# Optimization experiments

Hardware: AMD Instinct MI355X
Metric: run time of the kernel (lower is better)

## Reference

```python
import jax, jax.numpy as jnp
from jax import lax
import numpy as np

T, B, H = 128, 4096, 64

def setup_inputs() -> dict:
    key = jax.random.key(0)
    ks = jax.random.split(key, 7)
    s = 1.0 / np.sqrt(H)
    Hseq = jax.random.normal(ks[0], (T, B, H), dtype=jnp.float32)
    # PyTorch nn.GRU params: weight_ih_l0 [3H,H], weight_hh_l0 [3H,H], biases [3H]; gate order r,z,n
    W_ih = jax.random.uniform(ks[1], (3 * H, H), jnp.float32, -s, s)
    W_hh = jax.random.uniform(ks[2], (3 * H, H), jnp.float32, -s, s)
    b_ih = jax.random.uniform(ks[3], (3 * H,), jnp.float32, -s, s)
    b_hh = jax.random.uniform(ks[4], (3 * H,), jnp.float32, -s, s)
    W_out = jax.random.uniform(ks[5], (1, H), jnp.float32, -s, s)
    b_out = jax.random.uniform(ks[6], (1,), jnp.float32, -s, s)
    return {"Hseq": Hseq, "W_ih": W_ih, "W_hh": W_hh, "b_ih": b_ih, "b_hh": b_hh, "W_out": W_out, "b_out": b_out}

def reference(Hseq, W_ih, W_hh, b_ih, b_hh, W_out, b_out):
    # Precompute all input-side gate projections in one big GEMM: [T,B,3H]
    x_gates = jnp.einsum('tbh,gh->tbg', Hseq, W_ih) + b_ih

    def step(h, xg):
        hg = h @ W_hh.T + b_hh                     # [B,3H]
        xr, xz, xn = jnp.split(xg, 3, axis=-1)
        hr, hz, hn = jnp.split(hg, 3, axis=-1)
        r = jax.nn.sigmoid(xr + hr)
        z = jax.nn.sigmoid(xz + hz)
        n = jnp.tanh(xn + r * hn)
        h_new = (1.0 - z) * n + z * h
        return h_new, None

    h0 = jnp.zeros(Hseq.shape[1:], Hseq.dtype)      # [B,H], PyTorch default h0=0
    last, _ = lax.scan(step, h0, x_gates)           # last hidden == Y[-1]
    return (last @ W_out.T + b_out).squeeze(-1)     # [B]
```

## Files before the change

kernel.cpp:

```cpp
#include <hip/hip_runtime.h>
#include <stdint.h>

#define TT 128
#define BB 4096
#define HH 64
#define BC 16
#define XSTR 196
#define HSTR 72

typedef __attribute__((ext_vector_type(8))) short bf16x8;
typedef __attribute__((ext_vector_type(4))) float f32x4;

static __device__ __forceinline__ short f2bf(float f) {
  uint32_t u = __builtin_bit_cast(uint32_t, f);
  u += 0x7fffu + ((u >> 16) & 1u);
  return (short)(u >> 16);
}
static __device__ __forceinline__ uint32_t cvtpk(float a, float b) {
  uint32_t r;
  asm("v_cvt_pk_bf16_f32 %0, %1, %2" : "=v"(r) : "v"(a), "v"(b));
  return r;
}
static __device__ __forceinline__ float rcpf(float x) { return __builtin_amdgcn_rcpf(x); }
static __device__ __forceinline__ float sigm(float x) { return rcpf(1.0f + __expf(-x)); }
static __device__ __forceinline__ float tanhf_fast(float x) {
  float e = __expf(2.0f * x);
  return 1.0f - 2.0f * rcpf(e + 1.0f);
}

static __device__ __forceinline__ void block_sync_lds() {
  asm volatile("" ::: "memory");
  asm volatile("s_waitcnt lgkmcnt(0)" ::: "memory");
  __builtin_amdgcn_s_barrier();
  asm volatile("" ::: "memory");
}

#define MFMA __builtin_amdgcn_mfma_f32_16x16x32_bf16

__global__ __launch_bounds__(512) void gru_fused(
    const float* __restrict__ Hseq, const float* __restrict__ W_ih,
    const float* __restrict__ W_hh, const float* __restrict__ b_ih,
    const float* __restrict__ b_hh, const float* __restrict__ W_out,
    const float* __restrict__ b_out, float* __restrict__ out) {
  __shared__ __align__(16) short hsh[2][BC][HSTR];
  __shared__ __align__(16) float xgsh[4][BC][XSTR];
  __shared__ float psum[4][BC];

  const int tid = threadIdx.x;
  const int w   = tid >> 6;
  const int gw  = w & 3;
  const bool cons = (w < 4);
  const int l   = tid & 63;
  const int llo = l & 15;
  const int lhi = l >> 4;
  const int k0  = lhi * 8;
  const int bbase = blockIdx.x * BC;
  const f32x4 fz = {0.f, 0.f, 0.f, 0.f};

  for (int i = tid; i < BC * HSTR; i += 512) ((short*)hsh[0])[i] = 0;

  bf16x8 wa[3][2];
  f32x4 biasHN = fz;
  f32x4 biasPR = fz, biasPZ = fz, biasPN = fz;

  if (cons) {
#pragma unroll
    for (int c = 0; c < 3; ++c) {
      const int grow = 16 * gw + 64 * c + llo;
#pragma unroll
      for (int hf = 0; hf < 2; ++hf) {
        const float* q = &W_hh[grow * 64 + hf * 32 + k0];
        bf16x8 b;
#pragma unroll
        for (int i = 0; i < 8; ++i) b[i] = f2bf(q[i]);
        wa[c][hf] = b;
      }
    }
#pragma unroll
    for (int r = 0; r < 4; ++r) biasHN[r] = b_hh[128 + 16 * gw + 4 * lhi + r];
  } else {
#pragma unroll
    for (int c = 0; c < 3; ++c) {
      const int grow = 16 * gw + 64 * c + llo;
#pragma unroll
      for (int hf = 0; hf < 2; ++hf) {
        const float* p = &W_ih[grow * 64 + hf * 32 + k0];
        bf16x8 a;
#pragma unroll
        for (int i = 0; i < 8; ++i) a[i] = f2bf(p[i]);
        wa[c][hf] = a;
      }
    }
#pragma unroll
    for (int r = 0; r < 4; ++r) {
      const int j = 16 * gw + 4 * lhi + r;
      biasPR[r] = b_ih[j] + b_hh[j];
      biasPZ[r] = b_ih[64 + j] + b_hh[64 + j];
      biasPN[r] = b_ih[128 + j];
    }
  }

  const float* xroot = Hseq + (size_t)(bbase + llo) * HH + k0;
  f32x4 xqA0, xqA1, xqA2, xqA3, xqB0, xqB1, xqB2, xqB3;
  f32x4 hfp = fz;
  f32x4 xgE0, xgE1, xgE2, xgO0, xgO1, xgO2;

  if (!cons) {
#pragma unroll
    for (int s = 0; s < 2; ++s) {
      const f32x4* pv = (const f32x4*)(xroot + (size_t)s * BB * HH);
      f32x4 q0 = pv[0], q1 = pv[1], q2 = pv[8], q3 = pv[9];
      union { uint32_t u[4]; bf16x8 v; } c0, c1;
      c0.u[0] = cvtpk(q0[0], q0[1]); c0.u[1] = cvtpk(q0[2], q0[3]);
      c0.u[2] = cvtpk(q1[0], q1[1]); c0.u[3] = cvtpk(q1[2], q1[3]);
      c1.u[0] = cvtpk(q2[0], q2[1]); c1.u[1] = cvtpk(q2[2], q2[3]);
      c1.u[2] = cvtpk(q3[0], q3[1]); c1.u[3] = cvtpk(q3[2], q3[3]);
      f32x4 cR = biasPR, cZ = biasPZ, cN = biasPN;
      cR = MFMA(wa[0][0], c0.v, cR, 0, 0, 0);
      cR = MFMA(wa[0][1], c1.v, cR, 0, 0, 0);
      cZ = MFMA(wa[1][0], c0.v, cZ, 0, 0, 0);
      cZ = MFMA(wa[1][1], c1.v, cZ, 0, 0, 0);
      cN = MFMA(wa[2][0], c0.v, cN, 0, 0, 0);
      cN = MFMA(wa[2][1], c1.v, cN, 0, 0, 0);
      *(f32x4*)&xgsh[s][llo][16 * gw + 4 * lhi]       = cR;
      *(f32x4*)&xgsh[s][llo][64 + 16 * gw + 4 * lhi]  = cZ;
      *(f32x4*)&xgsh[s][llo][128 + 16 * gw + 4 * lhi] = cN;
    }
    const f32x4* pa = (const f32x4*)(xroot + (size_t)2 * BB * HH);
    xqA0 = pa[0]; xqA1 = pa[1]; xqA2 = pa[8]; xqA3 = pa[9];
    const f32x4* pb = (const f32x4*)(xroot + (size_t)3 * BB * HH);
    xqB0 = pb[0]; xqB1 = pb[1]; xqB2 = pb[8]; xqB3 = pb[9];
  }
  block_sync_lds();

  if (cons) {
    xgE0 = *(const f32x4*)&xgsh[0][llo][16 * gw + 4 * lhi];
    xgE1 = *(const f32x4*)&xgsh[0][llo][64 + 16 * gw + 4 * lhi];
    xgE2 = *(const f32x4*)&xgsh[0][llo][128 + 16 * gw + 4 * lhi];
  }

#define CSTEP(RBH, WBH, NB, XGC0, XGC1, XGC2, XGN0, XGN1, XGN2)               \
  {                                                                           \
    const bf16x8 hb0 = *(const bf16x8*)&hsh[RBH][llo][k0];                    \
    const bf16x8 hb1 = *(const bf16x8*)&hsh[RBH][llo][k0 + 32];               \
    XGN0 = *(const f32x4*)&xgsh[NB][llo][16 * gw + 4 * lhi];                  \
    XGN1 = *(const f32x4*)&xgsh[NB][llo][64 + 16 * gw + 4 * lhi];             \
    XGN2 = *(const f32x4*)&xgsh[NB][llo][128 + 16 * gw + 4 * lhi];            \
    f32x4 aR0 = MFMA(wa[0][0], hb0, XGC0, 0, 0, 0);                           \
    f32x4 aR1 = MFMA(wa[0][1], hb1, fz, 0, 0, 0);                             \
    f32x4 aZ  = MFMA(wa[1][0], hb0, XGC1, 0, 0, 0);                           \
    aZ        = MFMA(wa[1][1], hb1, aZ, 0, 0, 0);                             \
    f32x4 aHN = MFMA(wa[2][0], hb0, biasHN, 0, 0, 0);                         \
    aHN       = MFMA(wa[2][1], hb1, aHN, 0, 0, 0);                            \
    const f32x4 aR = aR0 + aR1;                                               \
    _Pragma("unroll")                                                         \
    for (int r = 0; r < 4; ++r) {                                             \
      const float rr = sigm(aR[r]);                                           \
      const float zz = sigm(aZ[r]);                                           \
      const float nn = tanhf_fast(XGC2[r] + rr * aHN[r]);                     \
      hfp[r] = nn + zz * (hfp[r] - nn);                                       \
    }                                                                         \
    uint2 pk;                                                                 \
    pk.x = cvtpk(hfp[0], hfp[1]);                                             \
    pk.y = cvtpk(hfp[2], hfp[3]);                                             \
    *(uint2*)&hsh[WBH][llo][16 * gw + 4 * lhi] = pk;                          \
  }

#define PSTEP(WRBUF, XQ0, XQ1, XQ2, XQ3, TN)                                  \
  {                                                                           \
    union { uint32_t u[4]; bf16x8 v; } c0, c1;                                \
    c0.u[0] = cvtpk(XQ0[0], XQ0[1]); c0.u[1] = cvtpk(XQ0[2], XQ0[3]);         \
    c0.u[2] = cvtpk(XQ1[0], XQ1[1]); c0.u[3] = cvtpk(XQ1[2], XQ1[3]);         \
    c1.u[0] = cvtpk(XQ2[0], XQ2[1]); c1.u[1] = cvtpk(XQ2[2], XQ2[3]);         \
    c1.u[2] = cvtpk(XQ3[0], XQ3[1]); c1.u[3] = cvtpk(XQ3[2], XQ3[3]);         \
    {                                                                         \
      const int tn = (TN) < TT ? (TN) : (TT - 1);                             \
      const f32x4* pv = (const f32x4*)(xroot + (size_t)tn * BB * HH);         \
      XQ0 = pv[0]; XQ1 = pv[1]; XQ2 = pv[8]; XQ3 = pv[9];                     \
    }                                                                         \
    f32x4 cR = biasPR, cZ = biasPZ, cN = biasPN;                              \
    cR = MFMA(wa[0][0], c0.v, cR, 0, 0, 0);                                   \
    cR = MFMA(wa[0][1], c1.v, cR, 0, 0, 0);                                   \
    cZ = MFMA(wa[1][0], c0.v, cZ, 0, 0, 0);                                   \
    cZ = MFMA(wa[1][1], c1.v, cZ, 0, 0, 0);                                   \
    cN = MFMA(wa[2][0], c0.v, cN, 0, 0, 0);                                   \
    cN = MFMA(wa[2][1], c1.v, cN, 0, 0, 0);                                   \
    *(f32x4*)&xgsh[WRBUF][llo][16 * gw + 4 * lhi]       = cR;                 \
    *(f32x4*)&xgsh[WRBUF][llo][64 + 16 * gw + 4 * lhi]  = cZ;                 \
    *(f32x4*)&xgsh[WRBUF][llo][128 + 16 * gw + 4 * lhi] = cN;                 \
  }

  for (int t = 0; t < TT; t += 4) {
    if (cons) { CSTEP(0, 1, 1, xgE0, xgE1, xgE2, xgO0, xgO1, xgO2) }
    else      { PSTEP(2, xqA0, xqA1, xqA2, xqA3, t + 4) }
    block_sync_lds();
    if (cons) { CSTEP(1, 0, 2, xgO0, xgO1, xgO2, xgE0, xgE1, xgE2) }
    else      { PSTEP(3, xqB0, xqB1, xqB2, xqB3, t + 5) }
    block_sync_lds();
    if (cons) { CSTEP(0, 1, 3, xgE0, xgE1, xgE2, xgO0, xgO1, xgO2) }
    else      { PSTEP(0, xqA0, xqA1, xqA2, xqA3, t + 6) }
    block_sync_lds();
    if (cons) { CSTEP(1, 0, 0, xgO0, xgO1, xgO2, xgE0, xgE1, xgE2) }
    else      { PSTEP(1, xqB0, xqB1, xqB2, xqB3, t + 7) }
    block_sync_lds();
  }
#undef CSTEP
#undef PSTEP

  if (cons) {
    float part = 0.f;
#pragma unroll
    for (int r = 0; r < 4; ++r) part += hfp[r] * W_out[16 * gw + 4 * lhi + r];
    part += __shfl_xor(part, 16);
    part += __shfl_xor(part, 32);
    if (lhi == 0) psum[gw][llo] = part;
  }
  block_sync_lds();
  if (tid < BC)
    out[bbase + tid] = psum[0][tid] + psum[1][tid] + psum[2][tid] + psum[3][tid] + b_out[0];
}

extern "C" void kernel_launch(void* const* d_in, const int* in_sizes, int n_in,
                              void* d_out, int out_size, void* d_ws, size_t ws_size,
                              hipStream_t stream) {
  (void)in_sizes; (void)n_in; (void)d_ws; (void)ws_size; (void)out_size;
  const float* Hseq  = (const float*)d_in[0];
  const float* W_ih  = (const float*)d_in[1];
  const float* W_hh  = (const float*)d_in[2];
  const float* b_ih  = (const float*)d_in[3];
  const float* b_hh  = (const float*)d_in[4];
  const float* W_out = (const float*)d_in[5];
  const float* b_out = (const float*)d_in[6];
  float* out = (float*)d_out;
  gru_fused<<<BB / BC, 512, 0, stream>>>(Hseq, W_ih, W_hh, b_ih, b_hh, W_out, b_out, out);
}
```

Baseline: 69.72 us.

## Replace per-step block barriers with LDS flag-based producer/consumer polling

Swaps the lockstep __syncthreads-style barriers between the producer waves (input projection) and the consumer waves (recurrent step) for per-wave progress flags in LDS that each side polls with s_sleep. Consumers wait only on the other three consumer waves' hidden-state flags and on their own producer's slot flag, so producers can run ahead by up to a ring of four xgate slots. The aim is to take the producer GEMM and the barrier overhead off the serial recurrence path. In exchange it adds polling latency and relies on volatile LDS ordering being correct without fences, which risks races.

```diff
diff --git a/kernel.cpp b/kernel.cpp
--- a/kernel.cpp
+++ b/kernel.cpp
@@ -27,12 +27,25 @@
   float e = __expf(2.0f * x);
   return 1.0f - 2.0f * rcpf(e + 1.0f);
 }
-
-static __device__ __forceinline__ void block_sync_lds() {
-  asm volatile("" ::: "memory");
+static __device__ __forceinline__ int imin2(int a, int b) { return a < b ? a : b; }
+
+static __device__ __forceinline__ void poll_min4(volatile int* f, int target) {
+  for (;;) {
+    const int a = f[0], b = f[1], c = f[2], d = f[3];
+    if (imin2(imin2(a, b), imin2(c, d)) >= target) break;
+    __builtin_amdgcn_s_sleep(1);
+  }
   asm volatile("s_waitcnt lgkmcnt(0)" ::: "memory");
-  __builtin_amdgcn_s_barrier();
-  asm volatile("" ::: "memory");
+}
+static __device__ __forceinline__ void poll_one(volatile int* f, int target) {
+  for (;;) {
+    if (*f >= target) break;
+    __builtin_amdgcn_s_sleep(1);
+  }
+  asm volatile("s_waitcnt lgkmcnt(0)" ::: "memory");
+}
+static __device__ __forceinline__ void lds_drain() {
+  asm volatile("s_waitcnt lgkmcnt(0)" ::: "memory");
 }
 
 #define MFMA __builtin_amdgcn_mfma_f32_16x16x32_bf16
@@ -45,6 +58,10 @@
   __shared__ __align__(16) short hsh[2][BC][HSTR];
   __shared__ __align__(16) float xgsh[4][BC][XSTR];
   __shared__ float psum[4][BC];
+  __shared__ int flagH[4];
+  __shared__ int flagP[4];
+  volatile int* vH = (volatile int*)flagH;
+  volatile int* vP = (volatile int*)flagP;
 
   const int tid = threadIdx.x;
   const int w   = tid >> 6;
@@ -57,6 +74,7 @@
   const int bbase = blockIdx.x * BC;
   const f32x4 fz = {0.f, 0.f, 0.f, 0.f};
 
+  if (tid < 4) { flagH[tid] = -1; flagP[tid] = -1; }
   for (int i = tid; i < BC * HSTR; i += 512) ((short*)hsh[0])[i] = 0;
 
   bf16x8 wa[3][2];
@@ -101,11 +119,12 @@
   }
 
   const float* xroot = Hseq + (size_t)(bbase + llo) * HH + k0;
-  f32x4 xqA0, xqA1, xqA2, xqA3, xqB0, xqB1, xqB2, xqB3;
   f32x4 hfp = fz;
-  f32x4 xgE0, xgE1, xgE2, xgO0, xgO1, xgO2;
+
+  __syncthreads();
 
   if (!cons) {
+    f32x4 xqA0, xqA1, xqA2, xqA3, xqB0, xqB1, xqB2, xqB3;
 #pragma unroll
     for (int s = 0; s < 2; ++s) {
       const f32x4* pv = (const f32x4*)(xroot + (size_t)s * BB * HH);
@@ -130,82 +149,84 @@
     xqA0 = pa[0]; xqA1 = pa[1]; xqA2 = pa[8]; xqA3 = pa[9];
     const f32x4* pb = (const f32x4*)(xroot + (size_t)3 * BB * HH);
     xqB0 = pb[0]; xqB1 = pb[1]; xqB2 = pb[8]; xqB3 = pb[9];
-  }
-  block_sync_lds();
-
-  if (cons) {
-    xgE0 = *(const f32x4*)&xgsh[0][llo][16 * gw + 4 * lhi];
-    xgE1 = *(const f32x4*)&xgsh[0][llo][64 + 16 * gw + 4 * lhi];
-    xgE2 = *(const f32x4*)&xgsh[0][llo][128 + 16 * gw + 4 * lhi];
-  }
-
-#define CSTEP(RBH, WBH, NB, XGC0, XGC1, XGC2, XGN0, XGN1, XGN2)               \
-  {                                                                           \
-    const bf16x8 hb0 = *(const bf16x8*)&hsh[RBH][llo][k0];                    \
-    const bf16x8 hb1 = *(const bf16x8*)&hsh[RBH][llo][k0 + 32];               \
-    XGN0 = *(const f32x4*)&xgsh[NB][llo][16 * gw + 4 * lhi];                  \
-    XGN1 = *(const f32x4*)&xgsh[NB][llo][64 + 16 * gw + 4 * lhi];             \
-    XGN2 = *(const f32x4*)&xgsh[NB][llo][128 + 16 * gw + 4 * lhi];            \
-    f32x4 aR0 = MFMA(wa[0][0], hb0, XGC0, 0, 0, 0);                           \
-    f32x4 aR1 = MFMA(wa[0][1], hb1, fz, 0, 0, 0);                             \
-    f32x4 aZ  = MFMA(wa[1][0], hb0, XGC1, 0, 0, 0);                           \
-    aZ        = MFMA(wa[1][1], hb1, aZ, 0, 0, 0);                             \
-    f32x4 aHN = MFMA(wa[2][0], hb0, biasHN, 0, 0, 0);                         \
-    aHN       = MFMA(wa[2][1], hb1, aHN, 0, 0, 0);                            \
-    const f32x4 aR = aR0 + aR1;                                               \
-    _Pragma("unroll")                                                         \
-    for (int r = 0; r < 4; ++r) {                                             \
-      const float rr = sigm(aR[r]);                                           \
-      const float zz = sigm(aZ[r]);                                           \
-      const float nn = tanhf_fast(XGC2[r] + rr * aHN[r]);                     \
-      hfp[r] = nn + zz * (hfp[r] - nn);                                       \
-    }                                                                         \
-    uint2 pk;                                                                 \
-    pk.x = cvtpk(hfp[0], hfp[1]);                                             \
-    pk.y = cvtpk(hfp[2], hfp[3]);                                             \
-    *(uint2*)&hsh[WBH][llo][16 * gw + 4 * lhi] = pk;                          \
-  }
-
-#define PSTEP(WRBUF, XQ0, XQ1, XQ2, XQ3, TN)                                  \
-  {                                                                           \
-    union { uint32_t u[4]; bf16x8 v; } c0, c1;                                \
-    c0.u[0] = cvtpk(XQ0[0], XQ0[1]); c0.u[1] = cvtpk(XQ0[2], XQ0[3]);         \
-    c0.u[2] = cvtpk(XQ1[0], XQ1[1]); c0.u[3] = cvtpk(XQ1[2], XQ1[3]);         \
-    c1.u[0] = cvtpk(XQ2[0], XQ2[1]); c1.u[1] = cvtpk(XQ2[2], XQ2[3]);         \
-    c1.u[2] = cvtpk(XQ3[0], XQ3[1]); c1.u[3] = cvtpk(XQ3[2], XQ3[3]);         \
+    lds_drain();
+    if (l == 0) vP[gw] = 1;
+
+#define PBODY(U, XQ0, XQ1, XQ2, XQ3)                                          \
     {                                                                         \
-      const int tn = (TN) < TT ? (TN) : (TT - 1);                             \
-      const f32x4* pv = (const f32x4*)(xroot + (size_t)tn * BB * HH);         \
-      XQ0 = pv[0]; XQ1 = pv[1]; XQ2 = pv[8]; XQ3 = pv[9];                     \
-    }                                                                         \
-    f32x4 cR = biasPR, cZ = biasPZ, cN = biasPN;                              \
-    cR = MFMA(wa[0][0], c0.v, cR, 0, 0, 0);                                   \
-    cR = MFMA(wa[0][1], c1.v, cR, 0, 0, 0);                                   \
-    cZ = MFMA(wa[1][0], c0.v, cZ, 0, 0, 0);                                   \
-    cZ = MFMA(wa[1][1], c1.v, cZ, 0, 0, 0);                                   \
-    cN = MFMA(wa[2][0], c0.v, cN, 0, 0, 0);                                   \
-    cN = MFMA(wa[2][1], c1.v, cN, 0, 0, 0);                                   \
-    *(f32x4*)&xgsh[WRBUF][llo][16 * gw + 4 * lhi]       = cR;                 \
-    *(f32x4*)&xgsh[WRBUF][llo][64 + 16 * gw + 4 * lhi]  = cZ;                 \
-    *(f32x4*)&xgsh[WRBUF][llo][128 + 16 * gw + 4 * lhi] = cN;                 \
-  }
-
-  for (int t = 0; t < TT; t += 4) {
-    if (cons) { CSTEP(0, 1, 1, xgE0, xgE1, xgE2, xgO0, xgO1, xgO2) }
-    else      { PSTEP(2, xqA0, xqA1, xqA2, xqA3, t + 4) }
-    block_sync_lds();
-    if (cons) { CSTEP(1, 0, 2, xgO0, xgO1, xgO2, xgE0, xgE1, xgE2) }
-    else      { PSTEP(3, xqB0, xqB1, xqB2, xqB3, t + 5) }
-    block_sync_lds();
-    if (cons) { CSTEP(0, 1, 3, xgE0, xgE1, xgE2, xgO0, xgO1, xgO2) }
-    else      { PSTEP(0, xqA0, xqA1, xqA2, xqA3, t + 6) }
-    block_sync_lds();
-    if (cons) { CSTEP(1, 0, 0, xgO0, xgO1, xgO2, xgE0, xgE1, xgE2) }
-    else      { PSTEP(1, xqB0, xqB1, xqB2, xqB3, t + 7) }
-    block_sync_lds();
-  }
-#undef CSTEP
-#undef PSTEP
+      poll_min4(vH, (U) - 5);                                                 \
+      union { uint32_t u[4]; bf16x8 v; } c0, c1;                              \
+      c0.u[0] = cvtpk(XQ0[0], XQ0[1]); c0.u[1] = cvtpk(XQ0[2], XQ0[3]);       \
+      c0.u[2] = cvtpk(XQ1[0], XQ1[1]); c0.u[3] = cvtpk(XQ1[2], XQ1[3]);       \
+      c1.u[0] = cvtpk(XQ2[0], XQ2[1]); c1.u[1] = cvtpk(XQ2[2], XQ2[3]);       \
+      c1.u[2] = cvtpk(XQ3[0], XQ3[1]); c1.u[3] = cvtpk(XQ3[2], XQ3[3]);       \
+      {                                                                       \
+        const int tn = imin2((U) + 2, TT - 1);                                \
+        const f32x4* pv = (const f32x4*)(xroot + (size_t)tn * BB * HH);       \
+        XQ0 = pv[0]; XQ1 = pv[1]; XQ2 = pv[8]; XQ3 = pv[9];                   \
+      }                                                                       \
+      f32x4 cR = biasPR, cZ = biasPZ, cN = biasPN;                            \
+      cR = MFMA(wa[0][0], c0.v, cR, 0, 0, 0);                                 \
+      cR = MFMA(wa[0][1], c1.v, cR, 0, 0, 0);                                 \
+      cZ = MFMA(wa[1][0], c0.v, cZ, 0, 0, 0);                                 \
+      cZ = MFMA(wa[1][1], c1.v, cZ, 0, 0, 0);                                 \
+      cN = MFMA(wa[2][0], c0.v, cN, 0, 0, 0);                                 \
+      cN = MFMA(wa[2][1], c1.v, cN, 0, 0, 0);                                 \
+      const int sl = (U) & 3;                                                 \
+      *(f32x4*)&xgsh[sl][llo][16 * gw + 4 * lhi]       = cR;                  \
+      *(f32x4*)&xgsh[sl][llo][64 + 16 * gw + 4 * lhi]  = cZ;                  \
+      *(f32x4*)&xgsh[sl][llo][128 + 16 * gw + 4 * lhi] = cN;                  \
+      lds_drain();                                                            \
+      if (l == 0) vP[gw] = (U);                                               \
+    }
+
+    for (int u = 2; u < TT; u += 2) {
+      PBODY(u,     xqA0, xqA1, xqA2, xqA3)
+      PBODY(u + 1, xqB0, xqB1, xqB2, xqB3)
+    }
+#undef PBODY
+  } else {
+    poll_one(&vP[gw], 0);
+    f32x4 xc0 = *(const f32x4*)&xgsh[0][llo][16 * gw + 4 * lhi];
+    f32x4 xc1 = *(const f32x4*)&xgsh[0][llo][64 + 16 * gw + 4 * lhi];
+    f32x4 xc2 = *(const f32x4*)&xgsh[0][llo][128 + 16 * gw + 4 * lhi];
+
+    for (int t = 0; t < TT; ++t) {
+      poll_min4(vH, t - 1);
+      const bf16x8 hb0 = *(const bf16x8*)&hsh[t & 1][llo][k0];
+      const bf16x8 hb1 = *(const bf16x8*)&hsh[t & 1][llo][k0 + 32];
+      f32x4 aR  = MFMA(wa[0][0], hb0, xc0, 0, 0, 0);
+      aR        = MFMA(wa[0][1], hb1, aR, 0, 0, 0);
+      f32x4 aZ  = MFMA(wa[1][0], hb0, xc1, 0, 0, 0);
+      aZ        = MFMA(wa[1][1], hb1, aZ, 0, 0, 0);
+      f32x4 aHN = MFMA(wa[2][0], hb0, biasHN, 0, 0, 0);
+      aHN       = MFMA(wa[2][1], hb1, aHN, 0, 0, 0);
+      f32x4 xn0 = xc0, xn1 = xc1, xn2 = xc2;
+      if (t + 1 < TT) {
+        poll_one(&vP[gw], t + 1);
+        const int nb = (t + 1) & 3;
+        xn0 = *(const f32x4*)&xgsh[nb][llo][16 * gw + 4 * lhi];
+        xn1 = *(const f32x4*)&xgsh[nb][llo][64 + 16 * gw + 4 * lhi];
+        xn2 = *(const f32x4*)&xgsh[nb][llo][128 + 16 * gw + 4 * lhi];
+      }
+#pragma unroll
+      for (int r = 0; r < 4; ++r) {
+        const float rr = sigm(aR[r]);
+        const float zz = sigm(aZ[r]);
+        const float nn = tanhf_fast(xc2[r] + rr * aHN[r]);
+        hfp[r] = nn + zz * (hfp[r] - nn);
+      }
+      uint2 pk;
+      pk.x = cvtpk(hfp[0], hfp[1]);
+      pk.y = cvtpk(hfp[2], hfp[3]);
+      *(uint2*)&hsh[(t + 1) & 1][llo][16 * gw + 4 * lhi] = pk;
+      lds_drain();
+      if (l == 0) vH[w] = t;
+      xc0 = xn0; xc1 = xn1; xc2 = xn2;
+    }
+  }
+
+  __syncthreads();
 
   if (cons) {
     float part = 0.f;
@@ -215,7 +236,7 @@
     part += __shfl_xor(part, 32);
     if (lhi == 0) psum[gw][llo] = part;
   }
-  block_sync_lds();
+  __syncthreads();
   if (tid < BC)
     out[bbase + tid] = psum[0][tid] + psum[1][tid] + psum[2][tid] + psum[3][tid] + b_out[0];
 }
```

Result: slower. 87.02 us (+24.8%).
